# Kernel optimization log

Hardware: AMD Instinct MI355X
Metric: run time of the kernel (lower is better)

## Reference

```python
import jax, jax.numpy as jnp
from jax import lax
import numpy as np

B = 8
NC = 80               # num_classes / cls_out_channels
SCORE_THR = 0.01      # test_cfg.score_thr
IOU_THR = 0.65        # test_cfg.nms.iou_threshold
PRE_TOPK = 5000       # min(num_bboxes, 5000)
MAX_PER_IMG = 100     # keepTopK
LEVELS = [(80, 80, 8), (40, 40, 16), (20, 20, 32)]  # (H, W, stride)


def make_priors():
    # MlvlPointGenerator with_stride=True: [x*s, y*s, s, s]
    parts = []
    for H, W, s in LEVELS:
        ys, xs = jnp.meshgrid(jnp.arange(H, dtype=jnp.float32),
                              jnp.arange(W, dtype=jnp.float32), indexing='ij')
        st = jnp.full((H * W,), float(s), dtype=jnp.float32)
        parts.append(jnp.stack([xs.ravel() * s, ys.ravel() * s, st, st], -1))
    return jnp.concatenate(parts, 0)  # [N, 4]


def _flatten(t, c):
    # NCHW -> [B, H*W, c]
    return t.transpose(0, 2, 3, 1).reshape(t.shape[0], -1, c)


def _decode(priors, bp):
    # priors [N,4], bp [B,N,4] -> xyxy boxes [B,N,4]
    xys = bp[..., :2] * priors[:, 2:] + priors[:, :2]
    whs = jnp.exp(bp[..., 2:]) * priors[:, 2:]
    return jnp.concatenate([xys - whs / 2, xys + whs / 2], -1)


def _iou_one(box, boxes):
    # box [4] vs boxes [T,4]
    tl = jnp.maximum(box[:2], boxes[:, :2])
    br = jnp.minimum(box[2:], boxes[:, 2:])
    wh = jnp.clip(br - tl, 0.0)
    inter = wh[:, 0] * wh[:, 1]
    a1 = (box[2] - box[0]) * (box[3] - box[1])
    a2 = (boxes[:, 2] - boxes[:, 0]) * (boxes[:, 3] - boxes[:, 1])
    return inter / (a1 + a2 - inter + 1e-6)


def _nms_single(boxes, scores):
    # greedy NMS on one class: boxes [T,4], scores [T]
    s0 = jnp.where(scores > SCORE_THR, scores, -1.0)

    def step(s, _):
        i = jnp.argmax(s)
        best = s[i]
        iou = _iou_one(boxes[i], boxes)
        s = jnp.where(iou > IOU_THR, -1.0, s).at[i].set(-1.0)
        return s, (i, jnp.where(best > 0, best, -1.0))

    _, (idx, ks) = lax.scan(jax.checkpoint(step), s0, None, length=MAX_PER_IMG)
    return idx, ks  # [K] indices into boxes, [K] kept scores (-1 = invalid)


def _per_image(boxes, scores):
    # boxes [N,4], scores [N,C]
    top_s, top_i = lax.top_k(scores.T, PRE_TOPK)          # [C,T]
    top_b = boxes[top_i]                                   # [C,T,4]
    idx, ks = jax.vmap(_nms_single)(top_b, top_s)          # [C,K]
    cb = jnp.take_along_axis(top_b, idx[..., None], axis=1)  # [C,K,4]
    cids = jnp.broadcast_to(jnp.arange(NC, dtype=jnp.int32)[:, None], ks.shape)
    fs, sel = lax.top_k(ks.reshape(-1), MAX_PER_IMG)       # global keepTopK
    fb = cb.reshape(-1, 4)[sel]
    fc = cids.reshape(-1)[sel]
    valid = fs > 0
    num = jnp.sum(valid.astype(jnp.int32))
    return (num,
            jnp.where(valid[:, None], fb, 0.0),
            jnp.where(valid, fs, 0.0),
            jnp.where(valid, fc, -1))


def _forward(cls0, bbox0, obj0, cls1, bbox1, obj1, cls2, bbox2, obj2):
    cls = jnp.concatenate([_flatten(c, NC) for c in (cls0, cls1, cls2)], 1)
    bp = jnp.concatenate([_flatten(b, 4) for b in (bbox0, bbox1, bbox2)], 1)
    obj = jnp.concatenate([_flatten(o, 1)[..., 0] for o in (obj0, obj1, obj2)], 1)
    priors = make_priors()
    boxes = _decode(priors, bp)                            # [B,N,4]
    scores = jax.nn.sigmoid(cls) * jax.nn.sigmoid(obj)[..., None]  # [B,N,C]
    return jax.vmap(_per_image)(boxes, scores)


def setup_inputs() -> dict:
    key = jax.random.key(0)
    ks = jax.random.split(key, 9)
    specs = [("cls0", (B, NC, 80, 80)), ("bbox0", (B, 4, 80, 80)), ("obj0", (B, 1, 80, 80)),
             ("cls1", (B, NC, 40, 40)), ("bbox1", (B, 4, 40, 40)), ("obj1", (B, 1, 40, 40)),
             ("cls2", (B, NC, 20, 20)), ("bbox2", (B, 4, 20, 20)), ("obj2", (B, 1, 20, 20))]
    return {n: jax.random.normal(k, sh, dtype=jnp.float32) for k, (n, sh) in zip(ks, specs)}


def reference(cls0, bbox0, obj0, cls1, bbox1, obj1, cls2, bbox2, obj2):
    # returns (num_detected [B], proposals [B,100,4], scores [B,100], cls_id [B,100])
    return _forward(cls0, bbox0, obj0, cls1, bbox1, obj1, cls2, bbox2, obj2)
```

## Files before the change

### kernel.cpp

```cpp
#include <hip/hip_runtime.h>
#include <math.h>
#include <stdint.h>

#define NCLS   80
#define NPTS   8400
#define KEEP   100
#define PRETOPK 5000
#define NB     8
#define THRBITS 0x3C23D70Au
#define BASEK   0x3C000000u

#define TBS    512
#define CAPF   448
#define NEEDF  192u
#define MTX    256
#define NW4    2100

#define TBT    1024
#define NREGT  8
#define CAPT   512

__device__ __forceinline__ float sigmoidf_(float x) { return 1.0f / (1.0f + expf(-x)); }

__device__ __forceinline__ float4 decode_one(int n, int b,
        const float* bb0, const float* bb1, const float* bb2) {
    const float* bb; int base, HW, x, y; float s;
    if (n < 6400)      { bb = bb0; base = n;        HW = 6400; s = 8.f;  y = base / 80; x = base - y * 80; }
    else if (n < 8000) { bb = bb1; base = n - 6400; HW = 1600; s = 16.f; y = base / 40; x = base - y * 40; }
    else               { bb = bb2; base = n - 8000; HW = 400;  s = 32.f; y = base / 20; x = base - y * 20; }
    const float* p = bb + (size_t)b * 4 * HW + base;
    float v0 = p[0], v1 = p[HW], v2 = p[2 * HW], v3 = p[3 * HW];
    float cx = v0 * s + x * s, cy = v1 * s + y * s;
    float w = expf(v2) * s, h = expf(v3) * s;
    return make_float4(cx - 0.5f * w, cy - 0.5f * h, cx + 0.5f * w, cy + 0.5f * h);
}

__device__ __forceinline__ bool iou_gt(float4 a, float4 c) {
    float tlx = fmaxf(a.x, c.x), tly = fmaxf(a.y, c.y);
    float brx = fminf(a.z, c.z), bry = fminf(a.w, c.w);
    float w = fmaxf(brx - tlx, 0.f), h = fmaxf(bry - tly, 0.f);
    float inter = w * h;
    float a1 = (a.z - a.x) * (a.w - a.y);
    float a2 = (c.z - c.x) * (c.w - c.y);
    return inter / (a1 + a2 - inter + 1e-6f) > 0.65f;
}

__device__ __forceinline__ void scan_hist1024(const uint32_t* sHist, uint32_t need, uint32_t cap,
                                              uint32_t carry, uint32_t prefix, int shift,
                                              uint32_t* shr, int lane) {
    const uint4* hv = (const uint4*)sHist;
    uint4 q0 = hv[lane * 4], q1 = hv[lane * 4 + 1], q2 = hv[lane * 4 + 2], q3 = hv[lane * 4 + 3];
    uint32_t csum = q0.x + q0.y + q0.z + q0.w + q1.x + q1.y + q1.z + q1.w
                  + q2.x + q2.y + q2.z + q2.w + q3.x + q3.y + q3.z + q3.w;
    uint32_t suf = csum;
    #pragma unroll
    for (int d = 1; d < 64; d <<= 1) {
        uint32_t t = (uint32_t)__shfl_down((int)suf, d);
        if (lane + d < 64) suf += t;
    }
    unsigned long long m = __ballot(carry + suf >= need);
    if (!m) { if (lane == 0) { shr[1] = 0u; shr[0] = 0u; } return; }
    int l1 = 63 - __clzll(m);
    uint32_t carry2 = carry + (uint32_t)__shfl((int)suf, l1) - (uint32_t)__shfl((int)csum, l1);
    uint32_t c2 = (lane < 16) ? sHist[l1 * 16 + lane] : 0u;
    uint32_t suf2 = c2;
    #pragma unroll
    for (int d = 1; d < 16; d <<= 1) {
        uint32_t t = (uint32_t)__shfl_down((int)suf2, d);
        if (lane + d < 16) suf2 += t;
    }
    unsigned long long m2 = __ballot(lane < 16 && (carry2 + suf2 >= need));
    int t2 = m2 ? (63 - __clzll(m2)) : 0;
    uint32_t suf2L = (uint32_t)__shfl((int)suf2, t2);
    uint32_t c2L   = (uint32_t)__shfl((int)c2, t2);
    int bin = l1 * 16 + t2;
    uint32_t cAbove = carry2 + suf2L - c2L;
    uint32_t cntIncl = cAbove + c2L;
    if (lane == 0) {
        if (cntIncl <= cap) { shr[1] = 0u; shr[0] = prefix | ((uint32_t)bin << shift); }
        else { shr[1] = 1u; shr[2] = prefix | ((uint32_t)bin << shift); shr[3] = cAbove; }
    }
}

__device__ __forceinline__ void scan_hist64_final(const uint32_t* sHist, uint32_t need, uint32_t cap,
                                                  uint32_t carry, uint32_t prefix,
                                                  uint32_t* shr, int lane) {
    uint32_t c2 = sHist[lane];
    uint32_t suf2 = c2;
    #pragma unroll
    for (int d = 1; d < 64; d <<= 1) {
        uint32_t t = (uint32_t)__shfl_down((int)suf2, d);
        if (lane + d < 64) suf2 += t;
    }
    unsigned long long m2 = __ballot(carry + suf2 >= need);
    int t2 = m2 ? (63 - __clzll(m2)) : 0;
    uint32_t suf2L = (uint32_t)__shfl((int)suf2, t2);
    uint32_t c2L   = (uint32_t)__shfl((int)c2, t2);
    uint32_t cAbove = carry + suf2L - c2L;
    uint32_t cntIncl = cAbove + c2L;
    if (lane == 0) {
        shr[1] = 0u;
        shr[0] = (cntIncl <= cap) ? (prefix | (uint32_t)t2)
                                  : ((prefix | (uint32_t)t2) + 1u);
    }
}

__global__ __launch_bounds__(TBS, 6)
void select_nms(const float* __restrict__ cls0, const float* __restrict__ bb0,
                const float* __restrict__ o0,
                const float* __restrict__ cls1, const float* __restrict__ bb1,
                const float* __restrict__ o1,
                const float* __restrict__ cls2, const float* __restrict__ bb2,
                const float* __restrict__ o2,
                float* __restrict__ keptScore, float4* __restrict__ keptBox) {
    __shared__ __align__(16) uint32_t sKey[NPTS];
    __shared__ __align__(16) char uMem[8192];
    __shared__ uint32_t sKeyS[CAPF];
    __shared__ uint16_t sIdxS[CAPF];
    __shared__ __align__(16) float4 bBoxS[CAPF];
    __shared__ uint32_t shr[4];
    __shared__ unsigned long long sh64;

    uint32_t* sHist = (uint32_t*)uMem;
    unsigned long long* cPack = (unsigned long long*)(uMem + 4096);
    typedef unsigned long long ull4[4];
    ull4* colM = (ull4*)uMem;

    int bc = blockIdx.x;
    int b = bc & 7;
    int c = bc >> 3;
    int tid = threadIdx.x, lane = tid & 63;

    sHist[tid] = 0; sHist[tid + TBS] = 0;
    __syncthreads();
    uint4* sKey4 = (uint4*)sKey;
    #pragma unroll
    for (int i = 0; i < 5; ++i) {
        int w = tid + i * TBS;
        if (w < NW4) {
            int n = w << 2;
            const float* cp; const float* op;
            if (w < 1600)      { cp = cls0 + ((size_t)b * NCLS + c) * 6400 + n;          op = o0 + (size_t)b * 6400 + n; }
            else if (w < 2000) { cp = cls1 + ((size_t)b * NCLS + c) * 1600 + (n - 6400); op = o1 + (size_t)b * 1600 + (n - 6400); }
            else               { cp = cls2 + ((size_t)b * NCLS + c) * 400 + (n - 8000);  op = o2 + (size_t)b * 400 + (n - 8000); }
            float4 cv = *(const float4*)cp;
            float4 ov = *(const float4*)op;
            uint32_t k0 = __float_as_uint(sigmoidf_(cv.x) * sigmoidf_(ov.x));
            uint32_t k1 = __float_as_uint(sigmoidf_(cv.y) * sigmoidf_(ov.y));
            uint32_t k2 = __float_as_uint(sigmoidf_(cv.z) * sigmoidf_(ov.z));
            uint32_t k3 = __float_as_uint(sigmoidf_(cv.w) * sigmoidf_(ov.w));
            sKey4[w] = make_uint4(k0, k1, k2, k3);
            if (k0 > THRBITS) atomicAdd(&sHist[(k0 - BASEK) >> 16], 1u);
            if (k1 > THRBITS) atomicAdd(&sHist[(k1 - BASEK) >> 16], 1u);
            if (k2 > THRBITS) atomicAdd(&sHist[(k2 - BASEK) >> 16], 1u);
            if (k3 > THRBITS) atomicAdd(&sHist[(k3 - BASEK) >> 16], 1u);
        }
    }
    __syncthreads();

    uint32_t prefix = 0, carry = 0, Tsel = 0;
    const uint4* k4 = (const uint4*)sKey;
    for (int level = 0;; ++level) {
        if (tid < 64) {
            if (level < 2) scan_hist1024(sHist, NEEDF, CAPF, carry, prefix, level == 0 ? 16 : 6, shr, lane);
            else           scan_hist64_final(sHist, NEEDF, CAPF, carry, prefix, shr, lane);
        }
        __syncthreads();
        if (shr[1] == 0u) { Tsel = shr[0]; break; }
        prefix = shr[2]; carry = shr[3];
        int nl = level + 1;
        if (nl == 2) { if (tid < 64) sHist[tid] = 0; } else { sHist[tid] = 0; sHist[tid + TBS] = 0; }
        __syncthreads();
        #pragma unroll
        for (int i = 0; i < 5; ++i) {
            int w = tid + i * TBS;
            if (w < NW4) {
                uint4 q = k4[w];
                #pragma unroll
                for (int j = 0; j < 4; ++j) {
                    uint32_t k = (j == 0) ? q.x : (j == 1) ? q.y : (j == 2) ? q.z : q.w;
                    if (k > THRBITS) {
                        uint32_t kp = k - BASEK;
                        if (nl == 1) { if ((kp >> 16) == (prefix >> 16)) atomicAdd(&sHist[(kp >> 6) & 1023u], 1u); }
                        else         { if ((kp >> 6)  == (prefix >> 6))  atomicAdd(&sHist[kp & 63u], 1u); }
                    }
                }
            }
        }
        __syncthreads();
    }
    __syncthreads();
    if (tid == 0) shr[3] = 0u;
    __syncthreads();

    #pragma unroll
    for (int i = 0; i < 5; ++i) {
        int w = tid + i * TBS;
        if (w < NW4) {
            uint4 q = k4[w];
            int n = w << 2;
            #pragma unroll
            for (int j = 0; j < 4; ++j) {
                uint32_t k = (j == 0) ? q.x : (j == 1) ? q.y : (j == 2) ? q.z : q.w;
                if (k > THRBITS && (k - BASEK) >= Tsel) {
                    uint32_t s = atomicAdd(&shr[3], 1u);
                    if (s < CAPF) cPack[s] = ((unsigned long long)k << 32) | (uint32_t)(0xFFFFu - (n + j));
                }
            }
        }
    }
    __syncthreads();
    int cnt = (int)shr[3]; if (cnt > CAPF) cnt = CAPF;
    if (tid < 16) cPack[cnt + tid] = 0ull;
    __syncthreads();

    if (tid < ((cnt + 63) & ~63)) {
        bool h0 = tid < cnt;
        unsigned long long my = h0 ? cPack[tid] : 0ull;
        int r0 = 0;
        const ulonglong2* cp2 = (const ulonglong2*)cPack;
        int nb16 = (cnt + 15) >> 4;
        for (int jb = 0; jb < nb16; ++jb) {
            ulonglong2 p0 = cp2[jb * 8 + 0], p1 = cp2[jb * 8 + 1], p2 = cp2[jb * 8 + 2], p3 = cp2[jb * 8 + 3];
            ulonglong2 p4 = cp2[jb * 8 + 4], p5 = cp2[jb * 8 + 5], p6 = cp2[jb * 8 + 6], p7 = cp2[jb * 8 + 7];
            r0 += (p0.x > my) + (p0.y > my) + (p1.x > my) + (p1.y > my)
                + (p2.x > my) + (p2.y > my) + (p3.x > my) + (p3.y > my)
                + (p4.x > my) + (p4.y > my) + (p5.x > my) + (p5.y > my)
                + (p6.x > my) + (p6.y > my) + (p7.x > my) + (p7.y > my);
        }
        if (h0) {
            sKeyS[r0] = (uint32_t)(my >> 32);
            sIdxS[r0] = (uint16_t)(0xFFFFu - (uint32_t)(my & 0xFFFFu));
        }
    }
    __syncthreads();

    if (tid < cnt) bBoxS[tid] = decode_one(sIdxS[tid], b, bb0, bb1, bb2);
    __syncthreads();

    int lim = (cnt < MTX) ? cnt : MTX;
    #pragma unroll
    for (int pp = 0; pp < 2; ++pp) {
        int t2 = tid + pp * TBS;
        int cand = t2 & 255, rb = t2 >> 8;
        int j0 = rb << 6;
        unsigned long long m = 0ull;
        if (cand < lim && j0 + 63 > cand) {
            float4 bcx = bBoxS[cand];
            #pragma unroll 8
            for (int jj = 0; jj < 64; ++jj)
                if (iou_gt(bBoxS[j0 + jj], bcx)) m |= 1ull << jj;
            if (j0 <= cand) m &= ~((2ull << (cand - j0)) - 1ull);
        }
        colM[cand][rb] = m;
    }
    __syncthreads();

    float4 kb0 = make_float4(0.f, 0.f, 0.f, 0.f), kb1 = kb0;
    float ks0 = -1.0f, ks1 = -1.0f;
    int K = 0;
    if (tid < 64) {
        const ulonglong2* cm2 = (const ulonglong2*)colM;
        ulonglong2 a01 = cm2[lane * 2 + 0],        a23 = cm2[lane * 2 + 1];
        ulonglong2 b01 = cm2[(64 + lane) * 2 + 0],  b23 = cm2[(64 + lane) * 2 + 1];
        ulonglong2 c01 = cm2[(128 + lane) * 2 + 0], c23 = cm2[(128 + lane) * 2 + 1];
        ulonglong2 d01 = cm2[(192 + lane) * 2 + 0], d23 = cm2[(192 + lane) * 2 + 1];
        __builtin_amdgcn_s_setprio(1);
        unsigned long long U0, U1, U2, U3;
        U0 = (lim >= 64) ? ~0ull : ((lim > 0) ? ((1ull << lim) - 1) : 0ull);
        U1 = (lim >= 128) ? ~0ull : ((lim > 64) ? ((1ull << (lim - 64)) - 1) : 0ull);
        U2 = (lim >= 192) ? ~0ull : ((lim > 128) ? ((1ull << (lim - 128)) - 1) : 0ull);
        U3 = (lim >= 256) ? ~0ull : ((lim > 192) ? ((1ull << (lim - 192)) - 1) : 0ull);
        int kIA = -1, kIB = -1;
        while (K < KEEP) {
            int i;
            if (U0) i = (int)__ffsll(U0) - 1;
            else if (U1) i = 64 + (int)__ffsll(U1) - 1;
            else if (U2) i = 128 + (int)__ffsll(U2) - 1;
            else if (U3) i = 192 + (int)__ffsll(U3) - 1;
            else break;
            int src = i & 63;
            unsigned long long s0, s1, s2, s3;
            if (i < 64)       { s0 = __shfl(a01.x, src); s1 = __shfl(a01.y, src); s2 = __shfl(a23.x, src); s3 = __shfl(a23.y, src); }
            else if (i < 128) { s0 = __shfl(b01.x, src); s1 = __shfl(b01.y, src); s2 = __shfl(b23.x, src); s3 = __shfl(b23.y, src); }
            else if (i < 192) { s0 = __shfl(c01.x, src); s1 = __shfl(c01.y, src); s2 = __shfl(c23.x, src); s3 = __shfl(c23.y, src); }
            else              { s0 = __shfl(d01.x, src); s1 = __shfl(d01.y, src); s2 = __shfl(d23.x, src); s3 = __shfl(d23.y, src); }
            if (i < 64)       U0 &= ~(1ull << i);
            else if (i < 128) U1 &= ~(1ull << (i - 64));
            else if (i < 192) U2 &= ~(1ull << (i - 128));
            else              U3 &= ~(1ull << (i - 192));
            U0 &= ~s0; U1 &= ~s1; U2 &= ~s2; U3 &= ~s3;
            if (K < 64) { if (lane == K) kIA = i; }
            else        { if (lane == K - 64) kIB = i; }
            K++;
        }
        if (kIA >= 0) { kb0 = bBoxS[kIA]; ks0 = __uint_as_float(sKeyS[kIA]); }
        if (kIB >= 0) { kb1 = bBoxS[kIB]; ks1 = __uint_as_float(sKeyS[kIB]); }
        for (int i = lim; i < cnt && K < KEEP; ++i) {
            float4 bx = bBoxS[i];
            bool sup = false;
            if (lane < K)      sup = iou_gt(bx, kb0);
            if (64 + lane < K) sup = sup || iou_gt(bx, kb1);
            if (!__any(sup ? 1 : 0)) {
                float sc = __uint_as_float(sKeyS[i]);
                if (K < 64) { if (lane == K)      { kb0 = bx; ks0 = sc; } }
                else        { if (lane == K - 64) { kb1 = bx; ks1 = sc; } }
                K++;
            }
        }
        __builtin_amdgcn_s_setprio(0);
        if (lane == 0) {
            shr[0] = (uint32_t)K;
            shr[1] = (uint32_t)cnt;
            shr[2] = (cnt > 0) ? sKeyS[cnt - 1] : 0xFFFFFFFFu;
            shr[3] = (cnt > 0) ? (uint32_t)sIdxS[cnt - 1] : 0xFFFFFFFFu;
        }
    }
    __syncthreads();
    int Kall = (int)shr[0]; int e = (int)shr[1];
    uint32_t cK = shr[2], cI = shr[3];

    if (Kall < KEEP && e < PRETOPK) {
        for (;;) {
            if (tid == 0) sh64 = 0ull;
            __syncthreads();
            unsigned long long best = 0ull;
            for (int i = 0; i < 17; ++i) {
                int n = tid + i * TBS;
                if (n < NPTS) {
                    uint32_t k = sKey[n];
                    if (k > THRBITS && (k < cK || (k == cK && (uint32_t)n > cI))) {
                        unsigned long long v = ((unsigned long long)k << 32) | (unsigned long long)(NPTS - 1 - n);
                        if (v > best) best = v;
                    }
                }
            }
            if (best) atomicMax(&sh64, best);
            __syncthreads();
            unsigned long long bv = sh64;
            if (bv == 0ull) break;
            uint32_t k = (uint32_t)(bv >> 32);
            int n = NPTS - 1 - (int)(bv & 0xFFFFFFFFull);
            if (tid < 64) {
                float4 bx = decode_one(n, b, bb0, bb1, bb2);
                bool sup = false;
                if (lane < K)      sup = iou_gt(bx, kb0);
                if (64 + lane < K) sup = sup || iou_gt(bx, kb1);
                if (!__any(sup ? 1 : 0)) {
                    float sc = __uint_as_float(k);
                    if (K < 64) { if (lane == K)      { kb0 = bx; ks0 = sc; } }
                    else        { if (lane == K - 64) { kb1 = bx; ks1 = sc; } }
                    K++;
                }
                if (lane == 0) shr[0] = (uint32_t)K;
            }
            __syncthreads();
            Kall = (int)shr[0];
            e++; cK = k; cI = (uint32_t)n;
            if (Kall >= KEEP || e >= PRETOPK) break;
        }
    }

    if (tid < 64) {
        int off = (b * NCLS + c) * KEEP;
        float4 z = make_float4(0.f, 0.f, 0.f, 0.f);
        keptScore[off + lane] = (lane < K) ? ks0 : -1.0f;
        keptBox[off + lane]   = (lane < K) ? kb0 : z;
        if (64 + lane < KEEP) {
            keptScore[off + 64 + lane] = (64 + lane < K) ? ks1 : -1.0f;
            keptBox[off + 64 + lane]   = (64 + lane < K) ? kb1 : z;
        }
    }
}

__global__ __launch_bounds__(TBT)
void topk_out(const float* __restrict__ keptScore, const float4* __restrict__ keptBox,
              float* __restrict__ out) {
    __shared__ __align__(16) uint32_t sHist[1024];
    __shared__ __align__(16) unsigned long long cPackT[CAPT + 16];
    __shared__ uint32_t sKeyS[CAPT];
    __shared__ uint16_t sIdxS[CAPT];
    __shared__ uint32_t shr[4];
    int b = blockIdx.x, tid = threadIdx.x, lane = tid & 63;
    const int TOT = NCLS * KEEP;

    uint32_t rKey[NREGT];
    #pragma unroll
    for (int i = 0; i < NREGT; ++i) {
        int n = tid + i * TBT;
        uint32_t key = 0u;
        if (n < TOT) {
            float s = keptScore[b * TOT + n];
            key = (s > 0.f) ? __float_as_uint(s) : 0u;
        }
        rKey[i] = key;
    }

    uint32_t prefix = 0, carry = 0, Tsel = 0;
    for (int level = 0;; ++level) {
        __syncthreads();
        if (level == 2) { if (tid < 64) sHist[tid] = 0; } else sHist[tid] = 0;
        __syncthreads();
        #pragma unroll
        for (int i = 0; i < NREGT; ++i) {
            uint32_t k = rKey[i];
            if (k > 0u) {
                uint32_t kp = k - BASEK;
                if (level == 0) atomicAdd(&sHist[kp >> 16], 1u);
                else if (level == 1) { if ((kp >> 16) == (prefix >> 16)) atomicAdd(&sHist[(kp >> 6) & 1023u], 1u); }
                else { if ((kp >> 6) == (prefix >> 6)) atomicAdd(&sHist[kp & 63u], 1u); }
            }
        }
        __syncthreads();
        if (tid < 64) {
            if (level < 2) scan_hist1024(sHist, (uint32_t)KEEP, (uint32_t)CAPT, carry, prefix, level == 0 ? 16 : 6, shr, lane);
            else           scan_hist64_final(sHist, (uint32_t)KEEP, (uint32_t)CAPT, carry, prefix, shr, lane);
        }
        __syncthreads();
        if (shr[1] == 0u) { Tsel = shr[0]; break; }
        prefix = shr[2]; carry = shr[3];
    }
    __syncthreads();
    if (tid == 0) shr[3] = 0u;
    __syncthreads();
    #pragma unroll
    for (int i = 0; i < NREGT; ++i) {
        uint32_t k = rKey[i];
        if (k > 0u && (k - BASEK) >= Tsel) {
            uint32_t s = atomicAdd(&shr[3], 1u);
            if (s < CAPT) cPackT[s] = ((unsigned long long)k << 32) | (uint32_t)(0xFFFFu - (tid + i * TBT));
        }
    }
    __syncthreads();
    int cnt = (int)shr[3]; if (cnt > CAPT) cnt = CAPT;
    if (tid < 16) cPackT[cnt + tid] = 0ull;
    __syncthreads();

    if (tid < ((cnt + 63) & ~63)) {
        bool h0 = tid < cnt;
        unsigned long long my = h0 ? cPackT[tid] : 0ull;
        int r0 = 0;
        const ulonglong2* cp2 = (const ulonglong2*)cPackT;
        int nb16 = (cnt + 15) >> 4;
        for (int jb = 0; jb < nb16; ++jb) {
            ulonglong2 p0 = cp2[jb * 8 + 0], p1 = cp2[jb * 8 + 1], p2 = cp2[jb * 8 + 2], p3 = cp2[jb * 8 + 3];
            ulonglong2 p4 = cp2[jb * 8 + 4], p5 = cp2[jb * 8 + 5], p6 = cp2[jb * 8 + 6], p7 = cp2[jb * 8 + 7];
            r0 += (p0.x > my) + (p0.y > my) + (p1.x > my) + (p1.y > my)
                + (p2.x > my) + (p2.y > my) + (p3.x > my) + (p3.y > my)
                + (p4.x > my) + (p4.y > my) + (p5.x > my) + (p5.y > my)
                + (p6.x > my) + (p6.y > my) + (p7.x > my) + (p7.y > my);
        }
        if (h0) {
            sKeyS[r0] = (uint32_t)(my >> 32);
            sIdxS[r0] = (uint16_t)(0xFFFFu - (uint32_t)(my & 0xFFFFu));
        }
    }
    __syncthreads();

    if (tid < KEEP) {
        bool valid = tid < cnt;
        int fi = valid ? (int)sIdxS[tid] : 0;
        float sc = valid ? __uint_as_float(sKeyS[tid]) : 0.f;
        float4 bx = valid ? keptBox[b * TOT + fi] : make_float4(0.f, 0.f, 0.f, 0.f);
        float cls = valid ? (float)(fi / KEEP) : -1.0f;
        float* boxOut = out + NB + (b * KEEP + tid) * 4;
        boxOut[0] = bx.x; boxOut[1] = bx.y; boxOut[2] = bx.z; boxOut[3] = bx.w;
        out[NB + NB * KEEP * 4 + b * KEEP + tid] = sc;
        out[NB + NB * KEEP * 4 + NB * KEEP + b * KEEP + tid] = cls;
    }
    if (tid == 0) out[b] = (float)((cnt < KEEP) ? cnt : KEEP);
}

extern "C" void kernel_launch(void* const* d_in, const int* in_sizes, int n_in,
                              void* d_out, int out_size, void* d_ws, size_t ws_size,
                              hipStream_t stream) {
    const float* cls0 = (const float*)d_in[0];
    const float* bb0  = (const float*)d_in[1];
    const float* obj0 = (const float*)d_in[2];
    const float* cls1 = (const float*)d_in[3];
    const float* bb1  = (const float*)d_in[4];
    const float* obj1 = (const float*)d_in[5];
    const float* cls2 = (const float*)d_in[6];
    const float* bb2  = (const float*)d_in[7];
    const float* obj2 = (const float*)d_in[8];
    float* out = (float*)d_out;

    char* ws = (char*)d_ws;
    float*  keptScore = (float*)(ws);
    float4* keptBox   = (float4*)(ws + 256000);

    select_nms<<<NB * NCLS, TBS, 0, stream>>>(cls0, bb0, obj0, cls1, bb1, obj1,
                                              cls2, bb2, obj2, keptScore, keptBox);
    topk_out<<<NB, TBT, 0, stream>>>(keptScore, keptBox, out);
}
```

Before: 165.2 us.

## Fuse final top-k into NMS kernel via last-block-done counter; read suppression rows from LDS

Removes the separate topk_out launch. Each (image, class) block of select_nms increments a per-image global counter, and the last block to finish for an image runs the cross-class top-100 selection, reusing its shared memory. The greedy NMS loop now reads each suppression row straight from LDS instead of keeping all rows in registers and broadcasting them with shuffles. In exchange it adds a memset launch and threadfences, and the final top-k runs on 512 threads re-reading global scores at every radix level instead of 1024 threads holding them in registers.

```diff
diff --git a/kernel.cpp b/kernel.cpp
--- a/kernel.cpp
+++ b/kernel.cpp
@@ -15,9 +15,6 @@
 #define NEEDF  192u
 #define MTX    256
 #define NW4    2100
-
-#define TBT    1024
-#define NREGT  8
 #define CAPT   512
 
 __device__ __forceinline__ float sigmoidf_(float x) { return 1.0f / (1.0f + expf(-x)); }
@@ -112,7 +109,8 @@
                 const float* __restrict__ o1,
                 const float* __restrict__ cls2, const float* __restrict__ bb2,
                 const float* __restrict__ o2,
-                float* __restrict__ keptScore, float4* __restrict__ keptBox) {
+                float* __restrict__ keptScore, float4* __restrict__ keptBox,
+                uint32_t* __restrict__ gCnt, float* __restrict__ out) {
     __shared__ __align__(16) uint32_t sKey[NPTS];
     __shared__ __align__(16) char uMem[8192];
     __shared__ uint32_t sKeyS[CAPF];
@@ -260,11 +258,6 @@
     float ks0 = -1.0f, ks1 = -1.0f;
     int K = 0;
     if (tid < 64) {
-        const ulonglong2* cm2 = (const ulonglong2*)colM;
-        ulonglong2 a01 = cm2[lane * 2 + 0],        a23 = cm2[lane * 2 + 1];
-        ulonglong2 b01 = cm2[(64 + lane) * 2 + 0],  b23 = cm2[(64 + lane) * 2 + 1];
-        ulonglong2 c01 = cm2[(128 + lane) * 2 + 0], c23 = cm2[(128 + lane) * 2 + 1];
-        ulonglong2 d01 = cm2[(192 + lane) * 2 + 0], d23 = cm2[(192 + lane) * 2 + 1];
         __builtin_amdgcn_s_setprio(1);
         unsigned long long U0, U1, U2, U3;
         U0 = (lim >= 64) ? ~0ull : ((lim > 0) ? ((1ull << lim) - 1) : 0ull);
@@ -279,17 +272,13 @@
             else if (U2) i = 128 + (int)__ffsll(U2) - 1;
             else if (U3) i = 192 + (int)__ffsll(U3) - 1;
             else break;
-            int src = i & 63;
-            unsigned long long s0, s1, s2, s3;
-            if (i < 64)       { s0 = __shfl(a01.x, src); s1 = __shfl(a01.y, src); s2 = __shfl(a23.x, src); s3 = __shfl(a23.y, src); }
-            else if (i < 128) { s0 = __shfl(b01.x, src); s1 = __shfl(b01.y, src); s2 = __shfl(b23.x, src); s3 = __shfl(b23.y, src); }
-            else if (i < 192) { s0 = __shfl(c01.x, src); s1 = __shfl(c01.y, src); s2 = __shfl(c23.x, src); s3 = __shfl(c23.y, src); }
-            else              { s0 = __shfl(d01.x, src); s1 = __shfl(d01.y, src); s2 = __shfl(d23.x, src); s3 = __shfl(d23.y, src); }
+            ulonglong2 r01 = *(const ulonglong2*)&colM[i][0];
+            ulonglong2 r23 = *(const ulonglong2*)&colM[i][2];
             if (i < 64)       U0 &= ~(1ull << i);
             else if (i < 128) U1 &= ~(1ull << (i - 64));
             else if (i < 192) U2 &= ~(1ull << (i - 128));
             else              U3 &= ~(1ull << (i - 192));
-            U0 &= ~s0; U1 &= ~s1; U2 &= ~s2; U3 &= ~s3;
+            U0 &= ~r01.x; U1 &= ~r01.y; U2 &= ~r23.x; U3 &= ~r23.y;
             if (K < 64) { if (lane == K) kIA = i; }
             else        { if (lane == K - 64) kIB = i; }
             K++;
@@ -371,77 +360,79 @@
             keptBox[off + 64 + lane]   = (64 + lane < K) ? kb1 : z;
         }
     }
-}
-
-__global__ __launch_bounds__(TBT)
-void topk_out(const float* __restrict__ keptScore, const float4* __restrict__ keptBox,
-              float* __restrict__ out) {
-    __shared__ __align__(16) uint32_t sHist[1024];
-    __shared__ __align__(16) unsigned long long cPackT[CAPT + 16];
-    __shared__ uint32_t sKeyS[CAPT];
-    __shared__ uint16_t sIdxS[CAPT];
-    __shared__ uint32_t shr[4];
-    int b = blockIdx.x, tid = threadIdx.x, lane = tid & 63;
+
+    __threadfence();
+    __syncthreads();
+    if (tid == 0) {
+        uint32_t prev = atomicAdd(&gCnt[b], 1u);
+        shr[0] = (prev == (uint32_t)(NCLS - 1)) ? 1u : 0u;
+    }
+    __syncthreads();
+    if (shr[0] != 1u) return;
+    __threadfence();
+
     const int TOT = NCLS * KEEP;
-
-    uint32_t rKey[NREGT];
-    #pragma unroll
-    for (int i = 0; i < NREGT; ++i) {
-        int n = tid + i * TBT;
-        uint32_t key = 0u;
+    uint32_t* tHist = sKey;
+    unsigned long long* tPack = (unsigned long long*)(sKey + 1024);
+    uint32_t* tKeyS = sKey + 2080;
+    uint16_t* tIdxS = (uint16_t*)(sKey + 2592);
+    const float* ksBase = keptScore + (size_t)b * TOT;
+
+    uint32_t tprefix = 0, tcarry = 0, tTsel = 0;
+    for (int level = 0;; ++level) {
+        __syncthreads();
+        if (level == 2) { if (tid < 64) tHist[tid] = 0; } else { tHist[tid] = 0; tHist[tid + TBS] = 0; }
+        __syncthreads();
+        #pragma unroll
+        for (int i = 0; i < 16; ++i) {
+            int n = tid + i * TBS;
+            if (n < TOT) {
+                float s = ksBase[n];
+                if (s > 0.f) {
+                    uint32_t kp = __float_as_uint(s) - BASEK;
+                    if (level == 0) atomicAdd(&tHist[kp >> 16], 1u);
+                    else if (level == 1) { if ((kp >> 16) == (tprefix >> 16)) atomicAdd(&tHist[(kp >> 6) & 1023u], 1u); }
+                    else { if ((kp >> 6) == (tprefix >> 6)) atomicAdd(&tHist[kp & 63u], 1u); }
+                }
+            }
+        }
+        __syncthreads();
+        if (tid < 64) {
+            if (level < 2) scan_hist1024(tHist, (uint32_t)KEEP, (uint32_t)CAPT, tcarry, tprefix, level == 0 ? 16 : 6, shr, lane);
+            else           scan_hist64_final(tHist, (uint32_t)KEEP, (uint32_t)CAPT, tcarry, tprefix, shr, lane);
+        }
+        __syncthreads();
+        if (shr[1] == 0u) { tTsel = shr[0]; break; }
+        tprefix = shr[2]; tcarry = shr[3];
+    }
+    __syncthreads();
+    if (tid == 0) shr[3] = 0u;
+    __syncthreads();
+    #pragma unroll
+    for (int i = 0; i < 16; ++i) {
+        int n = tid + i * TBS;
         if (n < TOT) {
-            float s = keptScore[b * TOT + n];
-            key = (s > 0.f) ? __float_as_uint(s) : 0u;
-        }
-        rKey[i] = key;
-    }
-
-    uint32_t prefix = 0, carry = 0, Tsel = 0;
-    for (int level = 0;; ++level) {
-        __syncthreads();
-        if (level == 2) { if (tid < 64) sHist[tid] = 0; } else sHist[tid] = 0;
-        __syncthreads();
-        #pragma unroll
-        for (int i = 0; i < NREGT; ++i) {
-            uint32_t k = rKey[i];
-            if (k > 0u) {
-                uint32_t kp = k - BASEK;
-                if (level == 0) atomicAdd(&sHist[kp >> 16], 1u);
-                else if (level == 1) { if ((kp >> 16) == (prefix >> 16)) atomicAdd(&sHist[(kp >> 6) & 1023u], 1u); }
-                else { if ((kp >> 6) == (prefix >> 6)) atomicAdd(&sHist[kp & 63u], 1u); }
-            }
-        }
-        __syncthreads();
-        if (tid < 64) {
-            if (level < 2) scan_hist1024(sHist, (uint32_t)KEEP, (uint32_t)CAPT, carry, prefix, level == 0 ? 16 : 6, shr, lane);
-            else           scan_hist64_final(sHist, (uint32_t)KEEP, (uint32_t)CAPT, carry, prefix, shr, lane);
-        }
-        __syncthreads();
-        if (shr[1] == 0u) { Tsel = shr[0]; break; }
-        prefix = shr[2]; carry = shr[3];
-    }
-    __syncthreads();
-    if (tid == 0) shr[3] = 0u;
-    __syncthreads();
-    #pragma unroll
-    for (int i = 0; i < NREGT; ++i) {
-        uint32_t k = rKey[i];
-        if (k > 0u && (k - BASEK) >= Tsel) {
-            uint32_t s = atomicAdd(&shr[3], 1u);
-            if (s < CAPT) cPackT[s] = ((unsigned long long)k << 32) | (uint32_t)(0xFFFFu - (tid + i * TBT));
-        }
-    }
-    __syncthreads();
-    int cnt = (int)shr[3]; if (cnt > CAPT) cnt = CAPT;
-    if (tid < 16) cPackT[cnt + tid] = 0ull;
-    __syncthreads();
-
-    if (tid < ((cnt + 63) & ~63)) {
-        bool h0 = tid < cnt;
-        unsigned long long my = h0 ? cPackT[tid] : 0ull;
+            float s = ksBase[n];
+            if (s > 0.f) {
+                uint32_t k = __float_as_uint(s);
+                if ((k - BASEK) >= tTsel) {
+                    uint32_t sl = atomicAdd(&shr[3], 1u);
+                    if (sl < CAPT) tPack[sl] = ((unsigned long long)k << 32) | (uint32_t)(0xFFFFu - n);
+                }
+            }
+        }
+    }
+    __syncthreads();
+    int tcnt = (int)shr[3]; if (tcnt > CAPT) tcnt = CAPT;
+    if (tid < 16) tPack[tcnt + tid] = 0ull;
+    __syncthreads();
+
+    if (tid < ((tcnt + 63) & ~63)) {
+        bool h0 = tid < tcnt;
+        unsigned long long my = h0 ? tPack[tid] : 0ull;
         int r0 = 0;
-        const ulonglong2* cp2 = (const ulonglong2*)cPackT;
-        int nb16 = (cnt + 15) >> 4;
+        const ulonglong2* cp2 = (const ulonglong2*)tPack;
+        int nb16 = (tcnt + 15) >> 4;
         for (int jb = 0; jb < nb16; ++jb) {
             ulonglong2 p0 = cp2[jb * 8 + 0], p1 = cp2[jb * 8 + 1], p2 = cp2[jb * 8 + 2], p3 = cp2[jb * 8 + 3];
             ulonglong2 p4 = cp2[jb * 8 + 4], p5 = cp2[jb * 8 + 5], p6 = cp2[jb * 8 + 6], p7 = cp2[jb * 8 + 7];
@@ -451,24 +442,27 @@
                 + (p6.x > my) + (p6.y > my) + (p7.x > my) + (p7.y > my);
         }
         if (h0) {
-            sKeyS[r0] = (uint32_t)(my >> 32);
-            sIdxS[r0] = (uint16_t)(0xFFFFu - (uint32_t)(my & 0xFFFFu));
+            tKeyS[r0] = (uint32_t)(my >> 32);
+            tIdxS[r0] = (uint16_t)(0xFFFFu - (uint32_t)(my & 0xFFFFu));
         }
     }
     __syncthreads();
 
     if (tid < KEEP) {
-        bool valid = tid < cnt;
-        int fi = valid ? (int)sIdxS[tid] : 0;
-        float sc = valid ? __uint_as_float(sKeyS[tid]) : 0.f;
-        float4 bx = valid ? keptBox[b * TOT + fi] : make_float4(0.f, 0.f, 0.f, 0.f);
+        bool valid = tid < tcnt;
+        int fi = valid ? (int)tIdxS[tid] : 0;
+        float sc = valid ? __uint_as_float(tKeyS[tid]) : 0.f;
+        float4 bx = valid ? keptBox[(size_t)b * TOT + fi] : make_float4(0.f, 0.f, 0.f, 0.f);
         float cls = valid ? (float)(fi / KEEP) : -1.0f;
         float* boxOut = out + NB + (b * KEEP + tid) * 4;
         boxOut[0] = bx.x; boxOut[1] = bx.y; boxOut[2] = bx.z; boxOut[3] = bx.w;
         out[NB + NB * KEEP * 4 + b * KEEP + tid] = sc;
         out[NB + NB * KEEP * 4 + NB * KEEP + b * KEEP + tid] = cls;
     }
-    if (tid == 0) out[b] = (float)((cnt < KEEP) ? cnt : KEEP);
+    if (tid == 0) {
+        out[b] = (float)((tcnt < KEEP) ? tcnt : KEEP);
+        atomicExch(&gCnt[b], 0u);
+    }
 }
 
 extern "C" void kernel_launch(void* const* d_in, const int* in_sizes, int n_in,
@@ -486,10 +480,12 @@
     float* out = (float*)d_out;
 
     char* ws = (char*)d_ws;
-    float*  keptScore = (float*)(ws);
-    float4* keptBox   = (float4*)(ws + 256000);
-
+    float*    keptScore = (float*)(ws);
+    float4*   keptBox   = (float4*)(ws + 256000);
+    uint32_t* gCnt      = (uint32_t*)(ws + 1280000);
+
+    hipMemsetAsync(gCnt, 0, 64, stream);
     select_nms<<<NB * NCLS, TBS, 0, stream>>>(cls0, bb0, obj0, cls1, bb1, obj1,
-                                              cls2, bb2, obj2, keptScore, keptBox);
-    topk_out<<<NB, TBT, 0, stream>>>(keptScore, keptBox, out);
-}
+                                              cls2, bb2, obj2, keptScore, keptBox,
+                                              gCnt, out);
+}
```

Result: slower. 239.2 us (+44.7%).
